# Kernel tuning notes

Measured on AMD Instinct MI355X. Metric: run time of the kernel, lower is better.

The kernel has to match this reference:

```python
import jax, jax.numpy as jnp
import numpy as np

B, N, F = 128, 64, 64          # batch, nodes, node features
FE = [2 * F + 1, 256, 256, 96] # edge MLP: fe_in = 2*node_size + num_ef(=1 dist)
FN = [FE[-1] + F, 256, 64]     # node MLP: fe_out + node_size
ALPHA = 0.2

def _lin(key, fan_in, fan_out):
    kw, kb = jax.random.split(key)
    s = 1.0 / np.sqrt(fan_in)
    return (jax.random.normal(kw, (fan_in, fan_out), jnp.float32) * s,
            jax.random.normal(kb, (fan_out,), jnp.float32) * s)

def setup_inputs() -> dict:
    key = jax.random.key(0)
    ks = jax.random.split(key, 6)
    x = jax.random.normal(ks[0], (B, N, F), jnp.float32)
    fe_W0, fe_b0 = _lin(ks[1], FE[0], FE[1])
    fe_W1, fe_b1 = _lin(ks[2], FE[1], FE[2])
    fe_W2, fe_b2 = _lin(ks[3], FE[2], FE[3])
    fn_W0, fn_b0 = _lin(ks[4], FN[0], FN[1])
    fn_W1, fn_b1 = _lin(ks[5], FN[1], FN[2])
    return {"x": x,
            "fe_W0": fe_W0, "fe_b0": fe_b0, "fe_W1": fe_W1, "fe_b1": fe_b1,
            "fe_W2": fe_W2, "fe_b2": fe_b2,
            "fn_W0": fn_W0, "fn_b0": fn_b0, "fn_W1": fn_W1, "fn_b1": fn_b1}

def _lrelu(v):
    return jax.nn.leaky_relu(v, ALPHA)

def reference(x, fe_W0, fe_b0, fe_W1, fe_b1, fe_W2, fe_b2, fn_W0, fn_b0, fn_W1, fn_b1):
    b, n, f = x.shape
    # fully-connected pairwise edge features: x1[b,i,j]=x[b,i], x2[b,i,j]=x[b,j]
    xi = jnp.broadcast_to(x[:, :, None, :], (b, n, n, f))
    xj = jnp.broadcast_to(x[:, None, :, :], (b, n, n, f))
    diffs = xj - xi
    dists = jnp.linalg.norm(diffs + 1e-12, axis=-1, keepdims=True)  # all_ef distance
    A = jnp.concatenate([xi, xj, dists], axis=-1)                   # [B,N,N,2F+1]
    # edge MLP fe (final_linear=False -> leaky relu after every layer)
    h = _lrelu(A @ fe_W0 + fe_b0)
    h = _lrelu(h @ fe_W1 + fe_b1)
    h = _lrelu(h @ fe_W2 + fe_b2)                                   # [B,N,N,96]
    agg = jnp.sum(h, axis=2)                                        # sum over neighbors j
    y = jnp.concatenate([agg, x], axis=-1)                          # [B,N,160]
    # node MLP fn (final_linear=True -> last layer linear)
    y = _lrelu(y @ fn_W0 + fn_b0)
    y = y @ fn_W1 + fn_b1                                           # [B,N,64]
    return y
```

## Files before the change

### kernel.cpp

```cpp
#include <hip/hip_runtime.h>

#define ALPHA 0.2f

typedef __attribute__((ext_vector_type(8))) short short8;
typedef __attribute__((ext_vector_type(4))) float f32x4;
typedef __attribute__((ext_vector_type(2))) unsigned int u32x2;
typedef __attribute__((ext_vector_type(4))) unsigned int u32x4;

__device__ __forceinline__ short f2bf(float f) {
    unsigned u = __builtin_bit_cast(unsigned, f);
    u += 0x7fffu + ((u >> 16) & 1u);
    return (short)(u >> 16);
}
__device__ __forceinline__ unsigned pack2(float a, float b) {
    unsigned ua = __builtin_bit_cast(unsigned, a) + 0x8000u;
    unsigned ub = __builtin_bit_cast(unsigned, b) + 0x8000u;
    return (ua >> 16) | (ub & 0xffff0000u);
}
__device__ __forceinline__ float bf2f(short s) {
    return __builtin_bit_cast(float, ((unsigned)(unsigned short)s) << 16);
}
__device__ __forceinline__ float lrelu(float v) { return fmaxf(v, ALPHA * v); }

__global__ void prep_kernel(const float* __restrict__ feW0, const float* __restrict__ feW1,
                            const float* __restrict__ feW2, const float* __restrict__ fnW0,
                            const float* __restrict__ fnW1,
                            short* __restrict__ W1F, short* __restrict__ W2F,
                            short* __restrict__ W0uvF,
                            short* __restrict__ Wn0T, short* __restrict__ Wn1T)
{
    const int tid = blockIdx.x * blockDim.x + threadIdx.x;
    const int T = gridDim.x * blockDim.x;
    for (int t = tid; t < 65536; t += T) {
        int e = t & 7, lane = (t >> 3) & 63, ks = (t >> 9) & 7, mt = t >> 12;
        int feat = mt * 16 + (lane & 15), k = ks * 32 + (lane >> 4) * 8 + e;
        W1F[t] = f2bf(feW1[k * 256 + feat]);
    }
    for (int t = tid; t < 32768; t += T) {
        int e = t & 7, lane = (t >> 3) & 63, ks = (t >> 9) & 7, mt = t >> 12;
        int feat = mt * 16 + (lane & 15), k = ks * 32 + (lane >> 4) * 8 + e;
        W2F[t] = f2bf(feat < 96 ? feW2[k * 96 + feat] : 0.f);
    }
    for (int t = tid; t < 32768; t += T) {
        int e = t & 7, lane = (t >> 3) & 63, ks = (t >> 9) & 1, mt = t >> 10;
        int feat = mt * 16 + (lane & 15), k = ks * 32 + (lane >> 4) * 8 + e;
        float val = (feat < 256) ? feW0[k * 256 + feat] : feW0[(64 + k) * 256 + (feat - 256)];
        W0uvF[t] = f2bf(val);
    }
    for (int t = tid; t < 256 * 160; t += T) { int n = t / 160, k = t - n * 160; Wn0T[t] = f2bf(fnW0[k * 256 + n]); }
    for (int t = tid; t < 64 * 256; t += T) { int n = t >> 8, k = t & 255; Wn1T[t] = f2bf(fnW1[k * 64 + n]); }
}

__global__ __launch_bounds__(256, 4)
void uv_kernel(const float* __restrict__ x, const short* __restrict__ W0uvF,
               float* __restrict__ u, float* __restrict__ v)
{
    __shared__ __align__(16) short xb[4096];
    const int tid = threadIdx.x;
    const int lane = tid & 63, wid = tid >> 6;
    const int l15 = lane & 15, lg = lane >> 4;
    const int r0 = blockIdx.x * 64;

    for (int t = tid; t < 4096; t += 256) {
        int row = t >> 6;
        int byte = (t * 2) ^ ((row & 7) << 4);
        *(short*)((char*)xb + byte) = f2bf(x[r0 * 64 + t]);
    }
    __syncthreads();

    #pragma unroll
    for (int pair = 0; pair < 4; ++pair) {
        const int mt0 = wid * 8 + pair * 2;
        f32x4 acc[2][4];
        #pragma unroll
        for (int m = 0; m < 2; ++m)
            #pragma unroll
            for (int nt = 0; nt < 4; ++nt) acc[m][nt] = (f32x4){0.f, 0.f, 0.f, 0.f};
        #pragma unroll
        for (int ks = 0; ks < 2; ++ks) {
            short8 a[2], bf[4];
            #pragma unroll
            for (int m = 0; m < 2; ++m)
                a[m] = *(const short8*)&W0uvF[(((mt0 + m) * 2 + ks) * 64 + lane) * 8];
            #pragma unroll
            for (int nt = 0; nt < 4; ++nt) {
                int row = nt * 16 + l15;
                int byte = (row * 128 + (ks * 32 + lg * 8) * 2) ^ ((row & 7) << 4);
                bf[nt] = *(const short8*)((char*)xb + byte);
            }
            #pragma unroll
            for (int m = 0; m < 2; ++m)
                #pragma unroll
                for (int nt = 0; nt < 4; ++nt)
                    acc[m][nt] = __builtin_amdgcn_mfma_f32_16x16x32_bf16(a[m], bf[nt], acc[m][nt], 0, 0, 0);
        }
        #pragma unroll
        for (int m = 0; m < 2; ++m) {
            int feat0 = (mt0 + m) * 16 + lg * 4;
            #pragma unroll
            for (int nt = 0; nt < 4; ++nt) {
                int R = r0 + nt * 16 + l15;
                float* dst = (feat0 < 256) ? &u[R * 256 + feat0] : &v[R * 256 + (feat0 - 256)];
                *(f32x4*)dst = acc[m][nt];
            }
        }
    }
}

__global__ __launch_bounds__(512, 2)
void edge_kernel(const float* __restrict__ x, const float* __restrict__ feW0,
                 const float* __restrict__ b0v, const float* __restrict__ b1v,
                 const float* __restrict__ b2v,
                 const short* __restrict__ W1F, const short* __restrict__ W2F,
                 const float* __restrict__ u, const float* __restrict__ v,
                 float* __restrict__ agg)
{
    __shared__ __align__(16) char smem[80384];
    char* h0 = smem;
    char* h1 = smem + 32768;
    short* ub_b = (short*)(smem + 65536);
    float* wd_f = (float*)(smem + 73728);
    float* dist = (float*)(smem + 74752);
    float* bb1s = (float*)(smem + 78848);
    float* bb2s = (float*)(smem + 79872);
    float* xs   = (float*)(smem + 32768);

    const int tid = threadIdx.x;
    const int lane = tid & 63, wid = tid >> 6;
    const int l15 = lane & 15, lg = lane >> 4;
    const int j8 = tid >> 3, p8 = tid & 7;
    const int b = blockIdx.x >> 2, i0 = (blockIdx.x & 3) * 16;
    const float* vbase = v + (size_t)b * 64 * 256;

    short8 a1[2][8];
    #pragma unroll
    for (int m = 0; m < 2; ++m)
        #pragma unroll
        for (int ks = 0; ks < 8; ++ks)
            a1[m][ks] = *(const short8*)&W1F[(((wid * 2 + m) * 8 + ks) * 64 + lane) * 8];
    short8 a2[8];
    #pragma unroll
    for (int ks = 0; ks < 8; ++ks)
        a2[ks] = *(const short8*)&W2F[((min(wid, 5) * 8 + ks) * 64 + lane) * 8];

    {
        const float* xb = x + b * 4096;
        *(f32x4*)&xs[j8 * 68 + p8 * 8]     = *(const f32x4*)&xb[j8 * 64 + p8 * 8];
        *(f32x4*)&xs[j8 * 68 + p8 * 8 + 4] = *(const f32x4*)&xb[j8 * 64 + p8 * 8 + 4];
    }
    {
        int ii = tid >> 5, c0 = (tid & 31) * 8;
        f32x4 u0 = *(const f32x4*)&u[(b * 64 + i0 + ii) * 256 + c0];
        f32x4 u1 = *(const f32x4*)&u[(b * 64 + i0 + ii) * 256 + c0 + 4];
        u0 += *(const f32x4*)&b0v[c0];
        u1 += *(const f32x4*)&b0v[c0 + 4];
        u32x4 pk;
        pk[0] = pack2(u0[0], u0[1]); pk[1] = pack2(u0[2], u0[3]);
        pk[2] = pack2(u1[0], u1[1]); pk[3] = pack2(u1[2], u1[3]);
        *(u32x4*)&ub_b[ii * 256 + c0] = pk;
    }
    if (tid < 64) {
        f32x4 w0 = *(const f32x4*)&feW0[128 * 256 + tid * 4];
        *(f32x4*)&wd_f[tid * 4] = w0;
    }
    if (tid < 256) bb1s[tid] = b1v[tid];
    else if (tid < 352) bb2s[tid - 256] = b2v[tid - 256];
    __syncthreads();

    {
        f32x4 xj0 = *(const f32x4*)&xs[j8 * 68 + p8 * 8];
        f32x4 xj1 = *(const f32x4*)&xs[j8 * 68 + p8 * 8 + 4];
        #pragma unroll
        for (int ii = 0; ii < 16; ++ii) {
            const float* xi = &xs[(i0 + ii) * 68 + p8 * 8];
            f32x4 xi0 = *(const f32x4*)&xi[0];
            f32x4 xi1 = *(const f32x4*)&xi[4];
            float ss = 0.f;
            #pragma unroll
            for (int r = 0; r < 4; ++r) {
                float d0 = xj0[r] - xi0[r] + 1e-12f;
                float d1 = xj1[r] - xi1[r] + 1e-12f;
                ss += d0 * d0 + d1 * d1;
            }
            ss += __shfl_xor(ss, 1); ss += __shfl_xor(ss, 2); ss += __shfl_xor(ss, 4);
            if (p8 == 0) dist[ii * 64 + j8] = sqrtf(ss);
        }
    }
    __syncthreads();

    #define BUILD(ii_) do { \
        float dj = dist[(ii_) * 64 + j8]; \
        const float* gv = vbase + j8 * 256 + p8 * 32; \
        _Pragma("unroll") \
        for (int e = 0; e < 4; ++e) { \
            int c0 = p8 * 32 + e * 8; \
            f32x4 va = *(const f32x4*)&gv[e * 8]; \
            f32x4 vb4 = *(const f32x4*)&gv[e * 8 + 4]; \
            short8 ur = *(const short8*)&ub_b[(ii_) * 256 + c0]; \
            f32x4 ww0 = *(const f32x4*)&wd_f[c0]; \
            f32x4 ww1 = *(const f32x4*)&wd_f[c0 + 4]; \
            float t0 = lrelu(bf2f(ur[0]) + va[0] + dj * ww0[0]); \
            float t1 = lrelu(bf2f(ur[1]) + va[1] + dj * ww0[1]); \
            float t2 = lrelu(bf2f(ur[2]) + va[2] + dj * ww0[2]); \
            float t3 = lrelu(bf2f(ur[3]) + va[3] + dj * ww0[3]); \
            float t4 = lrelu(bf2f(ur[4]) + vb4[0] + dj * ww1[0]); \
            float t5 = lrelu(bf2f(ur[5]) + vb4[1] + dj * ww1[1]); \
            float t6 = lrelu(bf2f(ur[6]) + vb4[2] + dj * ww1[2]); \
            float t7 = lrelu(bf2f(ur[7]) + vb4[3] + dj * ww1[3]); \
            u32x4 pk; \
            pk[0] = pack2(t0, t1); pk[1] = pack2(t2, t3); \
            pk[2] = pack2(t4, t5); pk[3] = pack2(t6, t7); \
            *(u32x4*)(h0 + ((j8 * 512 + c0 * 2) ^ ((j8 & 7) << 4))) = pk; \
        } \
    } while (0)

    BUILD(0);
    __syncthreads();

    float* aggrow = agg + (b * 64 + i0) * 96;
    for (int ii = 0; ii < 16; ++ii) {
        {
            f32x4 acc[2][4];
            #pragma unroll
            for (int m = 0; m < 2; ++m)
                #pragma unroll
                for (int nt = 0; nt < 4; ++nt) acc[m][nt] = (f32x4){0.f, 0.f, 0.f, 0.f};
            #pragma unroll
            for (int ks = 0; ks < 8; ++ks) {
                short8 bfr[4];
                #pragma unroll
                for (int nt = 0; nt < 4; ++nt) {
                    int j = nt * 16 + l15;
                    bfr[nt] = *(const short8*)(h0 + ((j * 512 + (ks * 32 + lg * 8) * 2) ^ ((j & 7) << 4)));
                }
                #pragma unroll
                for (int m = 0; m < 2; ++m)
                    #pragma unroll
                    for (int nt = 0; nt < 4; ++nt)
                        acc[m][nt] = __builtin_amdgcn_mfma_f32_16x16x32_bf16(a1[m][ks], bfr[nt], acc[m][nt], 0, 0, 0);
            }
            #pragma unroll
            for (int m = 0; m < 2; ++m) {
                int f0 = wid * 32 + m * 16 + lg * 4;
                f32x4 bb = *(const f32x4*)&bb1s[f0];
                #pragma unroll
                for (int nt = 0; nt < 4; ++nt) {
                    int j = nt * 16 + l15;
                    float q0 = lrelu(acc[m][nt][0] + bb[0]);
                    float q1 = lrelu(acc[m][nt][1] + bb[1]);
                    float q2 = lrelu(acc[m][nt][2] + bb[2]);
                    float q3 = lrelu(acc[m][nt][3] + bb[3]);
                    u32x2 pv; pv[0] = pack2(q0, q1); pv[1] = pack2(q2, q3);
                    *(u32x2*)(h1 + ((j * 512 + f0 * 2) ^ ((j & 7) << 4))) = pv;
                }
            }
        }
        __syncthreads();
        if (ii < 15) BUILD(ii + 1);
        if (wid < 6) {
            f32x4 acc2[4];
            #pragma unroll
            for (int nt = 0; nt < 4; ++nt) acc2[nt] = (f32x4){0.f, 0.f, 0.f, 0.f};
            #pragma unroll
            for (int ks = 0; ks < 8; ++ks) {
                #pragma unroll
                for (int nt = 0; nt < 4; ++nt) {
                    int j = nt * 16 + l15;
                    short8 bfr = *(const short8*)(h1 + ((j * 512 + (ks * 32 + lg * 8) * 2) ^ ((j & 7) << 4)));
                    acc2[nt] = __builtin_amdgcn_mfma_f32_16x16x32_bf16(a2[ks], bfr, acc2[nt], 0, 0, 0);
                }
            }
            const int f0 = wid * 16 + lg * 4;
            f32x4 bb = *(const f32x4*)&bb2s[f0];
            f32x4 s = (f32x4){0.f, 0.f, 0.f, 0.f};
            #pragma unroll
            for (int nt = 0; nt < 4; ++nt)
                #pragma unroll
                for (int r = 0; r < 4; ++r)
                    s[r] += lrelu(acc2[nt][r] + bb[r]);
            #pragma unroll
            for (int r = 0; r < 4; ++r) {
                float t = s[r];
                t += __shfl_xor(t, 1); t += __shfl_xor(t, 2);
                t += __shfl_xor(t, 4); t += __shfl_xor(t, 8);
                s[r] = t;
            }
            if (l15 == 0) *(f32x4*)&aggrow[ii * 96 + f0] = s;
        }
        __syncthreads();
    }
    #undef BUILD
}

__global__ __launch_bounds__(256, 2)
void node_kernel(const float* __restrict__ x, const float* __restrict__ agg,
                 const short* __restrict__ Wn0T, const short* __restrict__ Wn1T,
                 const float* __restrict__ bn0, const float* __restrict__ bn1,
                 float* __restrict__ out)
{
    __shared__ short A2[64 * 168];
    __shared__ short H[64 * 264];
    const int tid = threadIdx.x;
    const int lane = tid & 63, wid = tid >> 6;
    const int l15 = lane & 15, lg = lane >> 4;
    const int r0 = blockIdx.x * 64;

    for (int t = tid; t < 64 * 160; t += 256) {
        int j = t / 160, c = t - j * 160;
        float vv = (c < 96) ? agg[(r0 + j) * 96 + c] : x[(r0 + j) * 64 + (c - 96)];
        A2[j * 168 + c] = f2bf(vv);
    }
    __syncthreads();

    {
        f32x4 acc[4][4];
        #pragma unroll
        for (int mt = 0; mt < 4; ++mt)
            #pragma unroll
            for (int nt = 0; nt < 4; ++nt) acc[mt][nt] = (f32x4){0.f, 0.f, 0.f, 0.f};
        const int n0 = wid * 64;
        #pragma unroll
        for (int ks = 0; ks < 5; ++ks) {
            const int k0 = ks * 32 + lg * 8;
            short8 a[4], bf[4];
            #pragma unroll
            for (int mt = 0; mt < 4; ++mt)
                a[mt] = *reinterpret_cast<const short8*>(&A2[(mt * 16 + l15) * 168 + k0]);
            #pragma unroll
            for (int nt = 0; nt < 4; ++nt)
                bf[nt] = *reinterpret_cast<const short8*>(&Wn0T[(n0 + nt * 16 + l15) * 160 + k0]);
            #pragma unroll
            for (int mt = 0; mt < 4; ++mt)
                #pragma unroll
                for (int nt = 0; nt < 4; ++nt)
                    acc[mt][nt] = __builtin_amdgcn_mfma_f32_16x16x32_bf16(a[mt], bf[nt], acc[mt][nt], 0, 0, 0);
        }
        #pragma unroll
        for (int nt = 0; nt < 4; ++nt) {
            const int col = n0 + nt * 16 + l15;
            const float bv = bn0[col];
            #pragma unroll
            for (int mt = 0; mt < 4; ++mt)
                #pragma unroll
                for (int r = 0; r < 4; ++r)
                    H[(mt * 16 + lg * 4 + r) * 264 + col] = f2bf(lrelu(acc[mt][nt][r] + bv));
        }
    }
    __syncthreads();

    {
        f32x4 acc[4];
        #pragma unroll
        for (int mt = 0; mt < 4; ++mt) acc[mt] = (f32x4){0.f, 0.f, 0.f, 0.f};
        #pragma unroll
        for (int ks = 0; ks < 8; ++ks) {
            const int k0 = ks * 32 + lg * 8;
            short8 bf = *reinterpret_cast<const short8*>(&Wn1T[(wid * 16 + l15) * 256 + k0]);
            #pragma unroll
            for (int mt = 0; mt < 4; ++mt) {
                short8 a = *reinterpret_cast<const short8*>(&H[(mt * 16 + l15) * 264 + k0]);
                acc[mt] = __builtin_amdgcn_mfma_f32_16x16x32_bf16(a, bf, acc[mt], 0, 0, 0);
            }
        }
        const int col = wid * 16 + l15;
        const float bv = bn1[col];
        #pragma unroll
        for (int mt = 0; mt < 4; ++mt)
            #pragma unroll
            for (int r = 0; r < 4; ++r)
                out[(r0 + mt * 16 + lg * 4 + r) * 64 + col] = acc[mt][r] + bv;
    }
}

extern "C" void kernel_launch(void* const* d_in, const int* in_sizes, int n_in,
                              void* d_out, int out_size, void* d_ws, size_t ws_size,
                              hipStream_t stream) {
    (void)in_sizes; (void)n_in; (void)out_size; (void)ws_size;
    const float* x    = (const float*)d_in[0];
    const float* feW0 = (const float*)d_in[1];
    const float* feb0 = (const float*)d_in[2];
    const float* feW1 = (const float*)d_in[3];
    const float* feb1 = (const float*)d_in[4];
    const float* feW2 = (const float*)d_in[5];
    const float* feb2 = (const float*)d_in[6];
    const float* fnW0 = (const float*)d_in[7];
    const float* fnb0 = (const float*)d_in[8];
    const float* fnW1 = (const float*)d_in[9];
    const float* fnb1 = (const float*)d_in[10];

    char* ws = (char*)d_ws;
    short* W1F   = (short*)(ws + 0);
    short* W2F   = (short*)(ws + 131072);
    short* W0uvF = (short*)(ws + 196608);
    short* Wn0T  = (short*)(ws + 262144);
    short* Wn1T  = (short*)(ws + 344064);
    float* agg   = (float*)(ws + 376832);
    float* u     = (float*)(ws + 3522560);
    float* v     = (float*)(ws + 11911168);

    hipLaunchKernelGGL(prep_kernel, dim3(64), dim3(256), 0, stream,
                       feW0, feW1, feW2, fnW0, fnW1, W1F, W2F, W0uvF, Wn0T, Wn1T);
    hipLaunchKernelGGL(uv_kernel, dim3(128), dim3(256), 0, stream,
                       x, W0uvF, u, v);
    hipLaunchKernelGGL(edge_kernel, dim3(512), dim3(512), 0, stream,
                       x, feW0, feb0, feb1, feb2, W1F, W2F, u, v, agg);
    hipLaunchKernelGGL(node_kernel, dim3(128), dim3(256), 0, stream,
                       x, agg, Wn0T, Wn1T, fnb0, fnb1, (float*)d_out);
}
```

Measured before the change: 198.0 us.

## Halve edge tile to 32 neighbors per step to cut LDS and registers

Splits each node-i step of the edge kernel into two half-steps of 32 neighbors, halving the h0/h1 LDS buffers and the MFMA accumulator arrays. It also keeps the u+bias row in fp32 with an XOR swizzle instead of a bf16 copy. Total shared memory drops from about 80KB to about 56KB, which lowers LDS pressure and register use and may allow more resident blocks per CU. The cost is twice as many iterations and barriers, each doing half the MFMA work, so there is more synchronisation overhead.

```diff
diff --git a/kernel.cpp b/kernel.cpp
--- a/kernel.cpp
+++ b/kernel.cpp
@@ -115,20 +115,21 @@
                  const float* __restrict__ u, const float* __restrict__ v,
                  float* __restrict__ agg)
 {
-    __shared__ __align__(16) char smem[80384];
+    __shared__ __align__(16) char smem[55808];
     char* h0 = smem;
-    char* h1 = smem + 32768;
-    short* ub_b = (short*)(smem + 65536);
-    float* wd_f = (float*)(smem + 73728);
-    float* dist = (float*)(smem + 74752);
-    float* bb1s = (float*)(smem + 78848);
-    float* bb2s = (float*)(smem + 79872);
-    float* xs   = (float*)(smem + 32768);
+    char* h1 = smem + 16384;
+    float* ub_f = (float*)(smem + 32768);
+    float* wd_f = (float*)(smem + 49152);
+    float* dist = (float*)(smem + 50176);
+    float* bb1s = (float*)(smem + 54272);
+    float* bb2s = (float*)(smem + 55296);
+    float* xs   = (float*)smem;
 
     const int tid = threadIdx.x;
     const int lane = tid & 63, wid = tid >> 6;
     const int l15 = lane & 15, lg = lane >> 4;
     const int j8 = tid >> 3, p8 = tid & 7;
+    const int jr = tid >> 4, c16 = tid & 15;
     const int b = blockIdx.x >> 2, i0 = (blockIdx.x & 3) * 16;
     const float* vbase = v + (size_t)b * 64 * 256;
 
@@ -154,14 +155,13 @@
         f32x4 u1 = *(const f32x4*)&u[(b * 64 + i0 + ii) * 256 + c0 + 4];
         u0 += *(const f32x4*)&b0v[c0];
         u1 += *(const f32x4*)&b0v[c0 + 4];
-        u32x4 pk;
-        pk[0] = pack2(u0[0], u0[1]); pk[1] = pack2(u0[2], u0[3]);
-        pk[2] = pack2(u1[0], u1[1]); pk[3] = pack2(u1[2], u1[3]);
-        *(u32x4*)&ub_b[ii * 256 + c0] = pk;
+        int q = c0 >> 2;
+        *(f32x4*)&ub_f[(q ^ (q >> 3)) * 4 + ii * 256] = u0;
+        *(f32x4*)&ub_f[((q + 1) ^ ((q + 1) >> 3)) * 4 + ii * 256] = u1;
     }
     if (tid < 64) {
         f32x4 w0 = *(const f32x4*)&feW0[128 * 256 + tid * 4];
-        *(f32x4*)&wd_f[tid * 4] = w0;
+        *(f32x4*)&wd_f[(tid ^ (tid >> 3)) * 4] = w0;
     }
     if (tid < 256) bb1s[tid] = b1v[tid];
     else if (tid < 352) bb2s[tid - 256] = b2v[tid - 256];
@@ -188,29 +188,32 @@
     }
     __syncthreads();
 
-    #define BUILD(ii_) do { \
-        float dj = dist[(ii_) * 64 + j8]; \
-        const float* gv = vbase + j8 * 256 + p8 * 32; \
+    #define BUILD(s_) do { \
+        int jj = ((s_) & 1) * 32 + jr; \
+        float dj = dist[((s_) >> 1) * 64 + jj]; \
+        const float* gv = vbase + jj * 256 + c16 * 16; \
+        const float* ubrow = &ub_f[((s_) >> 1) * 256]; \
         _Pragma("unroll") \
-        for (int e = 0; e < 4; ++e) { \
-            int c0 = p8 * 32 + e * 8; \
-            f32x4 va = *(const f32x4*)&gv[e * 8]; \
-            f32x4 vb4 = *(const f32x4*)&gv[e * 8 + 4]; \
-            short8 ur = *(const short8*)&ub_b[(ii_) * 256 + c0]; \
-            f32x4 ww0 = *(const f32x4*)&wd_f[c0]; \
-            f32x4 ww1 = *(const f32x4*)&wd_f[c0 + 4]; \
-            float t0 = lrelu(bf2f(ur[0]) + va[0] + dj * ww0[0]); \
-            float t1 = lrelu(bf2f(ur[1]) + va[1] + dj * ww0[1]); \
-            float t2 = lrelu(bf2f(ur[2]) + va[2] + dj * ww0[2]); \
-            float t3 = lrelu(bf2f(ur[3]) + va[3] + dj * ww0[3]); \
-            float t4 = lrelu(bf2f(ur[4]) + vb4[0] + dj * ww1[0]); \
-            float t5 = lrelu(bf2f(ur[5]) + vb4[1] + dj * ww1[1]); \
-            float t6 = lrelu(bf2f(ur[6]) + vb4[2] + dj * ww1[2]); \
-            float t7 = lrelu(bf2f(ur[7]) + vb4[3] + dj * ww1[3]); \
+        for (int k = 0; k < 2; ++k) { \
+            f32x4 va = *(const f32x4*)&gv[k * 8]; \
+            f32x4 vb4 = *(const f32x4*)&gv[k * 8 + 4]; \
+            int q = c16 * 4 + k * 2; \
+            f32x4 uu0 = *(const f32x4*)&ubrow[(q ^ (q >> 3)) * 4]; \
+            f32x4 uu1 = *(const f32x4*)&ubrow[((q + 1) ^ ((q + 1) >> 3)) * 4]; \
+            f32x4 ww0 = *(const f32x4*)&wd_f[(q ^ (q >> 3)) * 4]; \
+            f32x4 ww1 = *(const f32x4*)&wd_f[((q + 1) ^ ((q + 1) >> 3)) * 4]; \
+            float t0 = lrelu(uu0[0] + va[0] + dj * ww0[0]); \
+            float t1 = lrelu(uu0[1] + va[1] + dj * ww0[1]); \
+            float t2 = lrelu(uu0[2] + va[2] + dj * ww0[2]); \
+            float t3 = lrelu(uu0[3] + va[3] + dj * ww0[3]); \
+            float t4 = lrelu(uu1[0] + vb4[0] + dj * ww1[0]); \
+            float t5 = lrelu(uu1[1] + vb4[1] + dj * ww1[1]); \
+            float t6 = lrelu(uu1[2] + vb4[2] + dj * ww1[2]); \
+            float t7 = lrelu(uu1[3] + vb4[3] + dj * ww1[3]); \
             u32x4 pk; \
             pk[0] = pack2(t0, t1); pk[1] = pack2(t2, t3); \
             pk[2] = pack2(t4, t5); pk[3] = pack2(t6, t7); \
-            *(u32x4*)(h0 + ((j8 * 512 + c0 * 2) ^ ((j8 & 7) << 4))) = pk; \
+            *(u32x4*)(h0 + ((jr * 512 + (c16 * 16 + k * 8) * 2) ^ ((jr & 7) << 4))) = pk; \
         } \
     } while (0)
 
@@ -218,25 +221,25 @@
     __syncthreads();
 
     float* aggrow = agg + (b * 64 + i0) * 96;
-    for (int ii = 0; ii < 16; ++ii) {
+    f32x4 sacc = (f32x4){0.f, 0.f, 0.f, 0.f};
+
+    for (int s = 0; s < 32; ++s) {
         {
-            f32x4 acc[2][4];
-            #pragma unroll
-            for (int m = 0; m < 2; ++m)
-                #pragma unroll
-                for (int nt = 0; nt < 4; ++nt) acc[m][nt] = (f32x4){0.f, 0.f, 0.f, 0.f};
+            f32x4 acc[2][2];
+            acc[0][0] = (f32x4){0.f,0.f,0.f,0.f}; acc[0][1] = (f32x4){0.f,0.f,0.f,0.f};
+            acc[1][0] = (f32x4){0.f,0.f,0.f,0.f}; acc[1][1] = (f32x4){0.f,0.f,0.f,0.f};
             #pragma unroll
             for (int ks = 0; ks < 8; ++ks) {
-                short8 bfr[4];
-                #pragma unroll
-                for (int nt = 0; nt < 4; ++nt) {
+                short8 bfr[2];
+                #pragma unroll
+                for (int nt = 0; nt < 2; ++nt) {
                     int j = nt * 16 + l15;
                     bfr[nt] = *(const short8*)(h0 + ((j * 512 + (ks * 32 + lg * 8) * 2) ^ ((j & 7) << 4)));
                 }
                 #pragma unroll
                 for (int m = 0; m < 2; ++m)
                     #pragma unroll
-                    for (int nt = 0; nt < 4; ++nt)
+                    for (int nt = 0; nt < 2; ++nt)
                         acc[m][nt] = __builtin_amdgcn_mfma_f32_16x16x32_bf16(a1[m][ks], bfr[nt], acc[m][nt], 0, 0, 0);
             }
             #pragma unroll
@@ -244,7 +247,7 @@
                 int f0 = wid * 32 + m * 16 + lg * 4;
                 f32x4 bb = *(const f32x4*)&bb1s[f0];
                 #pragma unroll
-                for (int nt = 0; nt < 4; ++nt) {
+                for (int nt = 0; nt < 2; ++nt) {
                     int j = nt * 16 + l15;
                     float q0 = lrelu(acc[m][nt][0] + bb[0]);
                     float q1 = lrelu(acc[m][nt][1] + bb[1]);
@@ -256,15 +259,14 @@
             }
         }
         __syncthreads();
-        if (ii < 15) BUILD(ii + 1);
+        if (s < 31) BUILD(s + 1);
         if (wid < 6) {
-            f32x4 acc2[4];
-            #pragma unroll
-            for (int nt = 0; nt < 4; ++nt) acc2[nt] = (f32x4){0.f, 0.f, 0.f, 0.f};
+            f32x4 acc2[2];
+            acc2[0] = (f32x4){0.f,0.f,0.f,0.f}; acc2[1] = (f32x4){0.f,0.f,0.f,0.f};
             #pragma unroll
             for (int ks = 0; ks < 8; ++ks) {
                 #pragma unroll
-                for (int nt = 0; nt < 4; ++nt) {
+                for (int nt = 0; nt < 2; ++nt) {
                     int j = nt * 16 + l15;
                     short8 bfr = *(const short8*)(h1 + ((j * 512 + (ks * 32 + lg * 8) * 2) ^ ((j & 7) << 4)));
                     acc2[nt] = __builtin_amdgcn_mfma_f32_16x16x32_bf16(a2[ks], bfr, acc2[nt], 0, 0, 0);
@@ -272,20 +274,20 @@
             }
             const int f0 = wid * 16 + lg * 4;
             f32x4 bb = *(const f32x4*)&bb2s[f0];
-            f32x4 s = (f32x4){0.f, 0.f, 0.f, 0.f};
-            #pragma unroll
-            for (int nt = 0; nt < 4; ++nt)
-                #pragma unroll
-                for (int r = 0; r < 4; ++r)
-                    s[r] += lrelu(acc2[nt][r] + bb[r]);
-            #pragma unroll
-            for (int r = 0; r < 4; ++r) {
-                float t = s[r];
-                t += __shfl_xor(t, 1); t += __shfl_xor(t, 2);
-                t += __shfl_xor(t, 4); t += __shfl_xor(t, 8);
-                s[r] = t;
-            }
-            if (l15 == 0) *(f32x4*)&aggrow[ii * 96 + f0] = s;
+            #pragma unroll
+            for (int r = 0; r < 4; ++r)
+                sacc[r] += lrelu(acc2[0][r] + bb[r]) + lrelu(acc2[1][r] + bb[r]);
+            if (s & 1) {
+                #pragma unroll
+                for (int r = 0; r < 4; ++r) {
+                    float t = sacc[r];
+                    t += __shfl_xor(t, 1); t += __shfl_xor(t, 2);
+                    t += __shfl_xor(t, 4); t += __shfl_xor(t, 8);
+                    sacc[r] = t;
+                }
+                if (l15 == 0) *(f32x4*)&aggrow[(s >> 1) * 96 + f0] = sacc;
+                sacc = (f32x4){0.f, 0.f, 0.f, 0.f};
+            }
         }
         __syncthreads();
     }
```

After: 185.9 us. 1.06x faster.

## Software-pipeline edge MLP layers with double-buffered LDS and one barrier per step

Applied to the files above, without the earlier changes.

The edge kernel now double-buffers both the layer-0 activation tile and the layer-1 output tile in LDS. Layer 2 for row s-1 runs in the same step as layer 1 for row s, which leaves one __syncthreads per iteration instead of two. The u-plus-bias rows are kept as fp32 in a swizzled layout instead of bf16, and the layer-2 weights are reloaded from global memory each step rather than held in registers. LDS use roughly doubles to about 150KB and launch bounds drop to one block per CU, trading occupancy for fewer barriers and better overlap.

```diff
diff --git a/kernel.cpp b/kernel.cpp
--- a/kernel.cpp
+++ b/kernel.cpp
@@ -16,9 +16,6 @@
     unsigned ua = __builtin_bit_cast(unsigned, a) + 0x8000u;
     unsigned ub = __builtin_bit_cast(unsigned, b) + 0x8000u;
     return (ua >> 16) | (ub & 0xffff0000u);
-}
-__device__ __forceinline__ float bf2f(short s) {
-    return __builtin_bit_cast(float, ((unsigned)(unsigned short)s) << 16);
 }
 __device__ __forceinline__ float lrelu(float v) { return fmaxf(v, ALPHA * v); }
 
@@ -107,7 +104,7 @@
     }
 }
 
-__global__ __launch_bounds__(512, 2)
+__global__ __launch_bounds__(512, 1)
 void edge_kernel(const float* __restrict__ x, const float* __restrict__ feW0,
                  const float* __restrict__ b0v, const float* __restrict__ b1v,
                  const float* __restrict__ b2v,
@@ -115,22 +112,20 @@
                  const float* __restrict__ u, const float* __restrict__ v,
                  float* __restrict__ agg)
 {
-    __shared__ __align__(16) char smem[80384];
-    char* h0 = smem;
-    char* h1 = smem + 32768;
-    short* ub_b = (short*)(smem + 65536);
-    float* wd_f = (float*)(smem + 73728);
-    float* dist = (float*)(smem + 74752);
-    float* bb1s = (float*)(smem + 78848);
-    float* bb2s = (float*)(smem + 79872);
-    float* xs   = (float*)(smem + 32768);
+    __shared__ __align__(16) char smem[154112];
+    float* ub_f = (float*)(smem + 131072);
+    float* wd_f = (float*)(smem + 147456);
+    float* dist = (float*)(smem + 148480);
+    float* bb1s = (float*)(smem + 152576);
+    float* bb2s = (float*)(smem + 153600);
+    float* xs   = (float*)(smem + 65536);
 
     const int tid = threadIdx.x;
     const int lane = tid & 63, wid = tid >> 6;
     const int l15 = lane & 15, lg = lane >> 4;
     const int j8 = tid >> 3, p8 = tid & 7;
     const int b = blockIdx.x >> 2, i0 = (blockIdx.x & 3) * 16;
-    const float* vbase = v + (size_t)b * 64 * 256;
+    const float* vbase = v + (size_t)b * 16384;
 
     short8 a1[2][8];
     #pragma unroll
@@ -138,10 +133,6 @@
         #pragma unroll
         for (int ks = 0; ks < 8; ++ks)
             a1[m][ks] = *(const short8*)&W1F[(((wid * 2 + m) * 8 + ks) * 64 + lane) * 8];
-    short8 a2[8];
-    #pragma unroll
-    for (int ks = 0; ks < 8; ++ks)
-        a2[ks] = *(const short8*)&W2F[((min(wid, 5) * 8 + ks) * 64 + lane) * 8];
 
     {
         const float* xb = x + b * 4096;
@@ -154,14 +145,13 @@
         f32x4 u1 = *(const f32x4*)&u[(b * 64 + i0 + ii) * 256 + c0 + 4];
         u0 += *(const f32x4*)&b0v[c0];
         u1 += *(const f32x4*)&b0v[c0 + 4];
-        u32x4 pk;
-        pk[0] = pack2(u0[0], u0[1]); pk[1] = pack2(u0[2], u0[3]);
-        pk[2] = pack2(u1[0], u1[1]); pk[3] = pack2(u1[2], u1[3]);
-        *(u32x4*)&ub_b[ii * 256 + c0] = pk;
+        int q = c0 >> 2;
+        *(f32x4*)&ub_f[(q ^ (q >> 3)) * 4 + ii * 256] = u0;
+        *(f32x4*)&ub_f[((q + 1) ^ ((q + 1) >> 3)) * 4 + ii * 256] = u1;
     }
     if (tid < 64) {
         f32x4 w0 = *(const f32x4*)&feW0[128 * 256 + tid * 4];
-        *(f32x4*)&wd_f[tid * 4] = w0;
+        *(f32x4*)&wd_f[(tid ^ (tid >> 3)) * 4] = w0;
     }
     if (tid < 256) bb1s[tid] = b1v[tid];
     else if (tid < 352) bb2s[tid - 256] = b2v[tid - 256];
@@ -188,38 +178,48 @@
     }
     __syncthreads();
 
-    #define BUILD(ii_) do { \
-        float dj = dist[(ii_) * 64 + j8]; \
-        const float* gv = vbase + j8 * 256 + p8 * 32; \
+    #define BUILD(t_, dst_) do { \
+        float dj = dist[(t_) * 64 + j8]; \
+        const float* gv = vbase + j8 * 256; \
+        const float* ubrow = &ub_f[(t_) * 256]; \
         _Pragma("unroll") \
         for (int e = 0; e < 4; ++e) { \
-            int c0 = p8 * 32 + e * 8; \
-            f32x4 va = *(const f32x4*)&gv[e * 8]; \
-            f32x4 vb4 = *(const f32x4*)&gv[e * 8 + 4]; \
-            short8 ur = *(const short8*)&ub_b[(ii_) * 256 + c0]; \
-            f32x4 ww0 = *(const f32x4*)&wd_f[c0]; \
-            f32x4 ww1 = *(const f32x4*)&wd_f[c0 + 4]; \
-            float t0 = lrelu(bf2f(ur[0]) + va[0] + dj * ww0[0]); \
-            float t1 = lrelu(bf2f(ur[1]) + va[1] + dj * ww0[1]); \
-            float t2 = lrelu(bf2f(ur[2]) + va[2] + dj * ww0[2]); \
-            float t3 = lrelu(bf2f(ur[3]) + va[3] + dj * ww0[3]); \
-            float t4 = lrelu(bf2f(ur[4]) + vb4[0] + dj * ww1[0]); \
-            float t5 = lrelu(bf2f(ur[5]) + vb4[1] + dj * ww1[1]); \
-            float t6 = lrelu(bf2f(ur[6]) + vb4[2] + dj * ww1[2]); \
-            float t7 = lrelu(bf2f(ur[7]) + vb4[3] + dj * ww1[3]); \
+            int c0 = e * 64 + p8 * 8; \
+            f32x4 va = *(const f32x4*)&gv[c0]; \
+            f32x4 vb4 = *(const f32x4*)&gv[c0 + 4]; \
+            int q0 = c0 >> 2; \
+            int s0 = (q0 ^ (q0 >> 3)) * 4, s1 = ((q0 + 1) ^ ((q0 + 1) >> 3)) * 4; \
+            f32x4 uu0 = *(const f32x4*)&ubrow[s0]; \
+            f32x4 uu1 = *(const f32x4*)&ubrow[s1]; \
+            f32x4 ww0 = *(const f32x4*)&wd_f[s0]; \
+            f32x4 ww1 = *(const f32x4*)&wd_f[s1]; \
+            float t0 = lrelu(uu0[0] + va[0] + dj * ww0[0]); \
+            float t1 = lrelu(uu0[1] + va[1] + dj * ww0[1]); \
+            float t2 = lrelu(uu0[2] + va[2] + dj * ww0[2]); \
+            float t3 = lrelu(uu0[3] + va[3] + dj * ww0[3]); \
+            float t4 = lrelu(uu1[0] + vb4[0] + dj * ww1[0]); \
+            float t5 = lrelu(uu1[1] + vb4[1] + dj * ww1[1]); \
+            float t6 = lrelu(uu1[2] + vb4[2] + dj * ww1[2]); \
+            float t7 = lrelu(uu1[3] + vb4[3] + dj * ww1[3]); \
             u32x4 pk; \
             pk[0] = pack2(t0, t1); pk[1] = pack2(t2, t3); \
             pk[2] = pack2(t4, t5); pk[3] = pack2(t6, t7); \
-            *(u32x4*)(h0 + ((j8 * 512 + c0 * 2) ^ ((j8 & 7) << 4))) = pk; \
+            *(u32x4*)((dst_) + ((j8 * 512 + c0 * 2) ^ ((j8 & 7) << 4))) = pk; \
         } \
     } while (0)
 
-    BUILD(0);
+    BUILD(0, smem);
     __syncthreads();
 
     float* aggrow = agg + (b * 64 + i0) * 96;
-    for (int ii = 0; ii < 16; ++ii) {
-        {
+
+    for (int s = 0; s <= 16; ++s) {
+        char* h0c = smem + ((s & 1) << 15);
+        char* h0n = smem + (((s + 1) & 1) << 15);
+        char* h1c = smem + 65536 + ((s & 1) << 15);
+        char* h1p = smem + 65536 + (((s + 1) & 1) << 15);
+
+        if (s < 16) {
             f32x4 acc[2][4];
             #pragma unroll
             for (int m = 0; m < 2; ++m)
@@ -231,7 +231,7 @@
                 #pragma unroll
                 for (int nt = 0; nt < 4; ++nt) {
                     int j = nt * 16 + l15;
-                    bfr[nt] = *(const short8*)(h0 + ((j * 512 + (ks * 32 + lg * 8) * 2) ^ ((j & 7) << 4)));
+                    bfr[nt] = *(const short8*)(h0c + ((j * 512 + (ks * 32 + lg * 8) * 2) ^ ((j & 7) << 4)));
                 }
                 #pragma unroll
                 for (int m = 0; m < 2; ++m)
@@ -251,13 +251,18 @@
                     float q2 = lrelu(acc[m][nt][2] + bb[2]);
                     float q3 = lrelu(acc[m][nt][3] + bb[3]);
                     u32x2 pv; pv[0] = pack2(q0, q1); pv[1] = pack2(q2, q3);
-                    *(u32x2*)(h1 + ((j * 512 + f0 * 2) ^ ((j & 7) << 4))) = pv;
+                    *(u32x2*)(h1c + ((j * 512 + f0 * 2) ^ ((j & 7) << 4))) = pv;
                 }
             }
         }
-        __syncthreads();
-        if (ii < 15) BUILD(ii + 1);
-        if (wid < 6) {
+
+        if (s + 1 < 16) BUILD(s + 1, h0n);
+
+        if (s >= 1 && wid < 6) {
+            short8 a2f[8];
+            #pragma unroll
+            for (int ks = 0; ks < 8; ++ks)
+                a2f[ks] = *(const short8*)&W2F[((wid * 8 + ks) * 64 + lane) * 8];
             f32x4 acc2[4];
             #pragma unroll
             for (int nt = 0; nt < 4; ++nt) acc2[nt] = (f32x4){0.f, 0.f, 0.f, 0.f};
@@ -266,27 +271,28 @@
                 #pragma unroll
                 for (int nt = 0; nt < 4; ++nt) {
                     int j = nt * 16 + l15;
-                    short8 bfr = *(const short8*)(h1 + ((j * 512 + (ks * 32 + lg * 8) * 2) ^ ((j & 7) << 4)));
-                    acc2[nt] = __builtin_amdgcn_mfma_f32_16x16x32_bf16(a2[ks], bfr, acc2[nt], 0, 0, 0);
+                    short8 bfr = *(const short8*)(h1p + ((j * 512 + (ks * 32 + lg * 8) * 2) ^ ((j & 7) << 4)));
+                    acc2[nt] = __builtin_amdgcn_mfma_f32_16x16x32_bf16(a2f[ks], bfr, acc2[nt], 0, 0, 0);
                 }
             }
             const int f0 = wid * 16 + lg * 4;
             f32x4 bb = *(const f32x4*)&bb2s[f0];
-            f32x4 s = (f32x4){0.f, 0.f, 0.f, 0.f};
+            f32x4 ssum = (f32x4){0.f, 0.f, 0.f, 0.f};
             #pragma unroll
             for (int nt = 0; nt < 4; ++nt)
                 #pragma unroll
                 for (int r = 0; r < 4; ++r)
-                    s[r] += lrelu(acc2[nt][r] + bb[r]);
+                    ssum[r] += lrelu(acc2[nt][r] + bb[r]);
             #pragma unroll
             for (int r = 0; r < 4; ++r) {
-                float t = s[r];
+                float t = ssum[r];
                 t += __shfl_xor(t, 1); t += __shfl_xor(t, 2);
                 t += __shfl_xor(t, 4); t += __shfl_xor(t, 8);
-                s[r] = t;
-            }
-            if (l15 == 0) *(f32x4*)&aggrow[ii * 96 + f0] = s;
-        }
+                ssum[r] = t;
+            }
+            if (l15 == 0) *(f32x4*)&aggrow[(s - 1) * 96 + f0] = ssum;
+        }
+
         __syncthreads();
     }
     #undef BUILD
```

Measured after the change: 165.0 us. -16.6%, faster.
